# Kernel optimization log

Hardware: AMD Instinct MI355X
Metric: run time of the kernel (lower is better)

The kernel has to match this reference:

```python
import jax, jax.numpy as jnp
import numpy as np

K = 32  # neighbors per point (self.k)

def setup_inputs() -> dict:
    key = jax.random.key(0)
    k1, k2 = jax.random.split(key)
    B, N, C = 16, 4096, 64
    x = jax.random.normal(k1, (B, N, C), dtype=jnp.float32)
    idx = jax.random.randint(k2, (B, N, K), 0, N, dtype=jnp.int64)
    return {"x": x, "idx": idx}

def reference(x, idx):
    # pooled[b, n, :] = mean_k x[b, idx[b, n, k], :]
    # gather per-batch: xb[ib] -> [N, K, C]
    gathered = jax.vmap(lambda xb, ib: xb[ib])(x, idx)  # [B, N, K, C]
    return gathered.mean(axis=2)  # [B, N, C]
```

## Files before the change

### kernel.cpp

```cpp
#include <hip/hip_runtime.h>


#define BB 16
#define NN 4096
#define KK 32
#define CC 64
#define CCH 4
#define NCHUNK (CC / CCH)
#define THREADS 512

__device__ __forceinline__ int detect_is64(const int* __restrict__ w) {
    int v = w[2 * (threadIdx.x & 63) + 1];
    return (__ballot(v != 0) == 0ULL) ? 1 : 0;
}

__global__ __launch_bounds__(256)
void pack_idx_kernel(const int* __restrict__ idx32,
                     ushort* __restrict__ out16) {
    const int is64 = detect_is64(idx32);
    const int tid = blockIdx.x * blockDim.x + threadIdx.x;
    const int stride = gridDim.x * blockDim.x;
    const int M = BB * NN * KK;
    if (is64) {
        const int4* __restrict__ in = (const int4*)idx32;
        uint* __restrict__ o = (uint*)out16;
        for (int i = tid; i < M / 2; i += stride) {
            int4 v = in[i];
            o[i] = (uint)(v.x & 0xFFFF) | ((uint)(v.z & 0xFFFF) << 16);
        }
    } else {
        const int4* __restrict__ in = (const int4*)idx32;
        uint2* __restrict__ o = (uint2*)out16;
        for (int i = tid; i < M / 4; i += stride) {
            int4 v = in[i];
            o[i] = make_uint2((uint)(v.x & 0xFFFF) | ((uint)(v.y & 0xFFFF) << 16),
                              (uint)(v.z & 0xFFFF) | ((uint)(v.w & 0xFFFF) << 16));
        }
    }
}

__global__ __launch_bounds__(THREADS)
void gapool_lds_kernel(const float* __restrict__ x,
                       const ushort* __restrict__ idx16,
                       float* __restrict__ out) {
    __shared__ float4 tile[NN];

    const int bid = blockIdx.x;
    const int b = bid & 15;
    const int chunk = bid >> 4;
    const int c0 = chunk * CCH;

    const float4* __restrict__ xb4 =
        (const float4*)(x + ((size_t)b * NN) * CC + c0);
    for (int n = threadIdx.x; n < NN; n += THREADS) {
        tile[n] = xb4[(size_t)n * (CC / 4)];
    }
    __syncthreads();

    const int wave = threadIdx.x >> 6;
    const int lane = threadIdx.x & 63;
    const int nwaves = THREADS >> 6;

    const float s = 1.0f / KK;

    for (int pg = wave; pg < NN / 64; pg += nwaves) {
        const int n = pg * 64 + lane;
        const size_t row = ((size_t)b * NN + n) * KK;

        const uint4* __restrict__ ip = (const uint4*)(idx16 + row);
        uint4 w0 = ip[0], w1 = ip[1], w2 = ip[2], w3 = ip[3];
        uint p[8] = {w0.x, w0.y, w0.z, w0.w, w1.x, w1.y, w1.z, w1.w};
        uint q[8] = {w2.x, w2.y, w2.z, w2.w, w3.x, w3.y, w3.z, w3.w};

        float4 acc0 = make_float4(0.f, 0.f, 0.f, 0.f);
        float4 acc1 = make_float4(0.f, 0.f, 0.f, 0.f);
#pragma unroll
        for (int i = 0; i < 8; ++i) {
            {
                float4 v = tile[p[i] & 0xFFFF];
                acc0.x += v.x; acc0.y += v.y; acc0.z += v.z; acc0.w += v.w;
            }
            {
                float4 v = tile[p[i] >> 16];
                acc1.x += v.x; acc1.y += v.y; acc1.z += v.z; acc1.w += v.w;
            }
            {
                float4 v = tile[q[i] & 0xFFFF];
                acc0.x += v.x; acc0.y += v.y; acc0.z += v.z; acc0.w += v.w;
            }
            {
                float4 v = tile[q[i] >> 16];
                acc1.x += v.x; acc1.y += v.y; acc1.z += v.z; acc1.w += v.w;
            }
        }

        float4 r = make_float4((acc0.x + acc1.x) * s, (acc0.y + acc1.y) * s,
                               (acc0.z + acc1.z) * s, (acc0.w + acc1.w) * s);
        *(float4*)(out + ((size_t)b * NN + n) * CC + c0) = r;
    }
}

extern "C" void kernel_launch(void* const* d_in, const int* in_sizes, int n_in,
                              void* d_out, int out_size, void* d_ws, size_t ws_size,
                              hipStream_t stream) {
    const float* x     = (const float*)d_in[0];
    const int*   idx32 = (const int*)d_in[1];
    float*       out   = (float*)d_out;
    ushort*      idx16 = (ushort*)d_ws;

    pack_idx_kernel<<<2048, 256, 0, stream>>>(idx32, idx16);

    gapool_lds_kernel<<<BB * NCHUNK, THREADS, 0, stream>>>(x, idx16, out);
}
```

Measured before the change: 90.51 us.

## Store LDS tile as per-channel planes and split points across two blocks

The gather kernel now keeps the x chunk in LDS as four scalar planes instead of float4 rows, so each neighbour lookup becomes four scalar LDS reads. The point range is also split across two blocks per (batch, chunk), doubling the grid to 512 blocks for better CU coverage, at the cost of each block reloading the full x chunk. The pack kernel grid is halved. Scalar planar reads may change the LDS bank-conflict pattern compared with 16-byte reads, but they issue four times as many LDS instructions.

```diff
diff --git a/kernel.cpp b/kernel.cpp
--- a/kernel.cpp
+++ b/kernel.cpp
@@ -7,6 +7,8 @@
 #define CC 64
 #define CCH 4
 #define NCHUNK (CC / CCH)
+#define NHALF 2
+#define PTS_PER_BLOCK (NN / NHALF)
 #define THREADS 512
 
 __device__ __forceinline__ int detect_is64(const int* __restrict__ w) {
@@ -40,62 +42,51 @@
 }
 
 __global__ __launch_bounds__(THREADS)
-void gapool_lds_kernel(const float* __restrict__ x,
-                       const ushort* __restrict__ idx16,
-                       float* __restrict__ out) {
-    __shared__ float4 tile[NN];
+void gapool_planar_kernel(const float* __restrict__ x,
+                          const ushort* __restrict__ idx16,
+                          float* __restrict__ out) {
+    __shared__ float plane[CCH][NN];
 
     const int bid = blockIdx.x;
     const int b = bid & 15;
-    const int chunk = bid >> 4;
+    const int g = bid >> 4;
+    const int chunk = g & (NCHUNK - 1);
+    const int half = g >> 4;
     const int c0 = chunk * CCH;
 
-    const float4* __restrict__ xb4 =
-        (const float4*)(x + ((size_t)b * NN) * CC + c0);
-    for (int n = threadIdx.x; n < NN; n += THREADS) {
-        tile[n] = xb4[(size_t)n * (CC / 4)];
+    const float* __restrict__ xb = x + ((size_t)b * NN) * CC + c0;
+    for (int r = threadIdx.x; r < NN; r += THREADS) {
+        const float4 v = *(const float4*)(xb + (size_t)r * CC);
+        plane[0][r] = v.x;
+        plane[1][r] = v.y;
+        plane[2][r] = v.z;
+        plane[3][r] = v.w;
     }
     __syncthreads();
 
-    const int wave = threadIdx.x >> 6;
-    const int lane = threadIdx.x & 63;
-    const int nwaves = THREADS >> 6;
-
+    const int n0 = half * PTS_PER_BLOCK;
     const float s = 1.0f / KK;
 
-    for (int pg = wave; pg < NN / 64; pg += nwaves) {
-        const int n = pg * 64 + lane;
-        const size_t row = ((size_t)b * NN + n) * KK;
+    for (int p = threadIdx.x; p < PTS_PER_BLOCK; p += THREADS) {
+        const int n = n0 + p;
+        const uint4* __restrict__ ip =
+            (const uint4*)(idx16 + ((size_t)b * NN + n) * KK);
+        const uint4 u0 = ip[0], u1 = ip[1], u2 = ip[2], u3 = ip[3];
+        const uint w[16] = {u0.x, u0.y, u0.z, u0.w, u1.x, u1.y, u1.z, u1.w,
+                            u2.x, u2.y, u2.z, u2.w, u3.x, u3.y, u3.z, u3.w};
 
-        const uint4* __restrict__ ip = (const uint4*)(idx16 + row);
-        uint4 w0 = ip[0], w1 = ip[1], w2 = ip[2], w3 = ip[3];
-        uint p[8] = {w0.x, w0.y, w0.z, w0.w, w1.x, w1.y, w1.z, w1.w};
-        uint q[8] = {w2.x, w2.y, w2.z, w2.w, w3.x, w3.y, w3.z, w3.w};
-
-        float4 acc0 = make_float4(0.f, 0.f, 0.f, 0.f);
-        float4 acc1 = make_float4(0.f, 0.f, 0.f, 0.f);
+        float a0 = 0.f, a1 = 0.f, a2 = 0.f, a3 = 0.f;
 #pragma unroll
-        for (int i = 0; i < 8; ++i) {
-            {
-                float4 v = tile[p[i] & 0xFFFF];
-                acc0.x += v.x; acc0.y += v.y; acc0.z += v.z; acc0.w += v.w;
-            }
-            {
-                float4 v = tile[p[i] >> 16];
-                acc1.x += v.x; acc1.y += v.y; acc1.z += v.z; acc1.w += v.w;
-            }
-            {
-                float4 v = tile[q[i] & 0xFFFF];
-                acc0.x += v.x; acc0.y += v.y; acc0.z += v.z; acc0.w += v.w;
-            }
-            {
-                float4 v = tile[q[i] >> 16];
-                acc1.x += v.x; acc1.y += v.y; acc1.z += v.z; acc1.w += v.w;
-            }
+        for (int i = 0; i < 16; ++i) {
+            const int j0 = (int)(w[i] & 0xFFFFu);
+            const int j1 = (int)(w[i] >> 16);
+            a0 += plane[0][j0]; a1 += plane[1][j0];
+            a2 += plane[2][j0]; a3 += plane[3][j0];
+            a0 += plane[0][j1]; a1 += plane[1][j1];
+            a2 += plane[2][j1]; a3 += plane[3][j1];
         }
 
-        float4 r = make_float4((acc0.x + acc1.x) * s, (acc0.y + acc1.y) * s,
-                               (acc0.z + acc1.z) * s, (acc0.w + acc1.w) * s);
+        float4 r = make_float4(a0 * s, a1 * s, a2 * s, a3 * s);
         *(float4*)(out + ((size_t)b * NN + n) * CC + c0) = r;
     }
 }
@@ -108,7 +99,8 @@
     float*       out   = (float*)d_out;
     ushort*      idx16 = (ushort*)d_ws;
 
-    pack_idx_kernel<<<2048, 256, 0, stream>>>(idx32, idx16);
+    pack_idx_kernel<<<1024, 256, 0, stream>>>(idx32, idx16);
 
-    gapool_lds_kernel<<<BB * NCHUNK, THREADS, 0, stream>>>(x, idx16, out);
+    gapool_planar_kernel<<<NHALF * NCHUNK * BB, THREADS, 0, stream>>>(
+        x, idx16, out);
 }
```

After: 106.2 us. 17.4% more time.
